# Performance work log

Hardware: AMD Instinct MI355X
Metric: run time of the kernel (lower is better)

## Reference

```python
import jax, jax.numpy as jnp
import numpy as np
from jax import lax

K = 5          # CARAFE kernel_size
S = 2          # scale_factor (downsample stride)
GROUP = 1      # mask groups
ENC_PAD = 1    # (encoder_kernel-1)*dilation//2 with encoder_kernel=3


def _conv2d(x, w, b, stride, padding, dilation=1):
    y = lax.conv_general_dilated(
        x, w, window_strides=(stride, stride),
        padding=[(padding, padding), (padding, padding)],
        rhs_dilation=(dilation, dilation),
        dimension_numbers=('NCHW', 'OIHW', 'NCHW'))
    return y + b[None, :, None, None]


def setup_inputs() -> dict:
    key = jax.random.key(0)
    k1, k2, k3 = jax.random.split(key, 3)
    B, C, H, W = 4, 256, 128, 128
    COMP = 64
    x = jax.random.normal(k1, (B, C, H, W), dtype=jnp.float32)
    # xavier-uniform-ish scale for compressor, std=0.001 for content encoder (as in init_weights)
    w1 = jax.random.normal(k2, (COMP, C, 1, 1), dtype=jnp.float32) * (1.0 / np.sqrt(C))
    b1 = jnp.zeros((COMP,), dtype=jnp.float32)
    w2 = jax.random.normal(k3, (K * K * GROUP, COMP, 3, 3), dtype=jnp.float32) * 0.001
    b2 = jnp.zeros((K * K * GROUP,), dtype=jnp.float32)
    return {"x": x, "w1": w1, "b1": b1, "w2": w2, "b2": b2}


def _carafe_forward(x, w1, b1, w2, b2):
    B, C, H, W = x.shape
    compressed = _conv2d(x, w1, b1, stride=1, padding=0)           # (B, 64, H, W)
    mask = _conv2d(compressed, w2, b2, stride=S, padding=ENC_PAD)   # (B, K*K*G, Ho, Wo)
    Ho, Wo = mask.shape[2], mask.shape[3]
    # kernel_normalizer: softmax over the K*K window per group
    mask = jax.nn.softmax(mask.reshape(B, GROUP, K * K, Ho, Wo), axis=2)
    # feature_reassemble: fused unfold * mask sum — accumulate per kernel tap to
    # avoid materializing the full (B, C, K*K, Ho, Wo) tensor.
    pad = K // 2
    x_pad = jnp.pad(x, ((0, 0), (0, 0), (pad, pad), (pad, pad)))
    Cg = C // GROUP
    out = jnp.zeros((B, GROUP, Cg, Ho, Wo), dtype=x.dtype)
    for i in range(K):
        for j in range(K):
            patch = x_pad[:, :, i:i + S * (Ho - 1) + 1:S, j:j + S * (Wo - 1) + 1:S]
            patch = patch.reshape(B, GROUP, Cg, Ho, Wo)
            out = out + patch * mask[:, :, i * K + j][:, :, None]
    return out.reshape(B, C, Ho, Wo)


def reference(x, w1, b1, w2, b2):
    return _carafe_forward(x, w1, b1, w2, b2)
```

## Files before the change

### kernel.cpp

```cpp
#include <hip/hip_runtime.h>
#include <math.h>

#define BN   4
#define CN   256
#define HN   128
#define WN   128
#define COMP 64
#define KK   25
#define HO   64
#define WO   64

#define TB_OFF    36864
#define PL_OFF    37120
#define PL_SLICE  (BN * HO * KK * 64)
#define XT_OFF    (PL_OFF + 2 * PL_SLICE)
#define WS_NEED   ((size_t)(XT_OFF + (size_t)BN * HN * WN * CN / 2) * 4)

typedef short v8s  __attribute__((ext_vector_type(8)));
typedef float v16f __attribute__((ext_vector_type(16)));

__device__ inline ushort f2bf(float f) {
  unsigned u = __float_as_uint(f);
  return (ushort)((u + 0x7fffu + ((u >> 16) & 1u)) >> 16);
}

__global__ __launch_bounds__(64) void compose_mfma(
    const float* __restrict__ w1, const float* __restrict__ b1,
    const float* __restrict__ w2, float* __restrict__ ws) {
  const int t = blockIdx.x, chunk = blockIdx.y;
  const int lane = threadIdx.x;
  const int m = lane & 31, half = lane >> 5;
  const int c0 = chunk * 16 + half * 8;
  float acc[8] = {0.f, 0.f, 0.f, 0.f, 0.f, 0.f, 0.f, 0.f};
  if (m < KK) {
    for (int k = 0; k < COMP; ++k) {
      float wv = w2[(size_t)(m * COMP + k) * 9 + t];
      const float* w1r = w1 + (size_t)k * CN + c0;
      float4 a = *(const float4*)w1r;
      float4 bq = *(const float4*)(w1r + 4);
      acc[0] += wv * a.x;  acc[1] += wv * a.y;
      acc[2] += wv * a.z;  acc[3] += wv * a.w;
      acc[4] += wv * bq.x; acc[5] += wv * bq.y;
      acc[6] += wv * bq.z; acc[7] += wv * bq.w;
    }
  }
  ushort* wA = (ushort*)ws;
  ushort pk[8];
#pragma unroll
  for (int j = 0; j < 8; ++j) pk[j] = f2bf(acc[j]);
  *(ushort4*)(wA + ((size_t)(t * 16 + chunk) * 64 + lane) * 8) =
      make_ushort4(pk[0], pk[1], pk[2], pk[3]);
  *(ushort4*)(wA + ((size_t)(t * 16 + chunk) * 64 + lane) * 8 + 4) =
      make_ushort4(pk[4], pk[5], pk[6], pk[7]);
  if (chunk == 0 && lane < KK) {
    float tbv = 0.f;
    for (int k = 0; k < COMP; ++k)
      tbv += w2[(size_t)(lane * COMP + k) * 9 + t] * b1[k];
    ws[TB_OFF + lane * 9 + t] = tbv;
  }
}

__global__ __launch_bounds__(256) void transpose_x(
    const float* __restrict__ x, float* __restrict__ ws) {
  __shared__ float st[64][65];
  const int wt = blockIdx.x & 1, ct = blockIdx.x >> 1;
  const int h = blockIdx.y, b = blockIdx.z;
  const int tid = threadIdx.x;
  const int w0 = wt * 64, c0 = ct * 64;
  {
    const int wl = tid & 63, cw = tid >> 6;
#pragma unroll
    for (int i = 0; i < 16; ++i) {
      int cl = cw * 16 + i;
      st[cl][wl] = x[((size_t)(b * CN + c0 + cl) * HN + h) * WN + w0 + wl];
    }
  }
  __syncthreads();
  ushort* xT = (ushort*)(ws + XT_OFF);
  const int cg = tid & 15, wl0 = tid >> 4;
#pragma unroll
  for (int wi = 0; wi < 4; ++wi) {
    int wl = wl0 + wi * 16;
    ushort4 o = make_ushort4(f2bf(st[cg * 4 + 0][wl]), f2bf(st[cg * 4 + 1][wl]),
                             f2bf(st[cg * 4 + 2][wl]), f2bf(st[cg * 4 + 3][wl]));
    *(ushort4*)(xT + ((size_t)((b * HN + h) * WN + w0 + wl)) * CN + c0 + cg * 4) = o;
  }
}

__global__ __launch_bounds__(64) void conv_mfma(
    const float* __restrict__ ws, float* __restrict__ pl) {
  const int wt = blockIdx.x & 1, z = blockIdx.x >> 1;
  const int ho = blockIdx.y, b = blockIdx.z;
  const int lane = threadIdx.x;
  const int n = lane & 31, half = lane >> 5;
  const int wo = wt * 32 + n;
  const ushort* xT = (const ushort*)(ws + XT_OFF);
  const ushort* wA = (const ushort*)ws;
  const int coff = z * 128 + half * 8;
  const v8s zero8 = {};
  v16f acc = {};

#pragma unroll
  for (int dr = 0; dr < 3; ++dr) {
    const int r = 2 * ho + dr - 1;
    if (r < 0) continue;
#pragma unroll
    for (int dc = 0; dc < 3; ++dc) {
      const int t = dr * 3 + dc;
      const int q = 2 * wo + dc - 1;
      const bool bad = q < 0;
      const int qc = bad ? 0 : q;
      const ushort* bp = xT + ((size_t)((b * HN + r) * WN + qc)) * CN + coff;
      const ushort* ap = wA + ((size_t)(t * 16 + z * 8) * 64 + lane) * 8;
      v8s bf[8], af[8];
#pragma unroll
      for (int cc = 0; cc < 8; ++cc) {
        bf[cc] = *(const v8s*)(bp + cc * 16);
        af[cc] = *(const v8s*)(ap + (size_t)cc * 512);
      }
      if (dc == 0) {
#pragma unroll
        for (int cc = 0; cc < 8; ++cc) bf[cc] = bad ? zero8 : bf[cc];
      }
#pragma unroll
      for (int cc = 0; cc < 8; ++cc)
        acc = __builtin_amdgcn_mfma_f32_32x32x16_bf16(af[cc], bf[cc], acc, 0, 0, 0);
    }
  }

  float* dst = pl + (size_t)z * PL_SLICE + ((size_t)(b * HO + ho) * KK) * 64 + wo;
#pragma unroll
  for (int rg = 0; rg < 16; ++rg) {
    int m = (rg & 3) + 8 * (rg >> 2) + 4 * half;
    if (m < KK) dst[(size_t)m * 64] = acc[rg];
  }
}

__global__ __launch_bounds__(1024, 4) void gather_kernel(
    const float* __restrict__ x, const float* __restrict__ b2,
    const float* __restrict__ tb, const float* __restrict__ pl,
    float* __restrict__ out) {
  const int ho  = blockIdx.x;
  const int b   = blockIdx.y;
  const int z   = blockIdx.z;
  const int tid = threadIdx.x;
  const int wo  = tid & 63;
  const int wv  = tid >> 6;
  const int c_base = __builtin_amdgcn_readfirstlane(z * (CN / 2) + wv * 8);

  __shared__ float sm[KK * 64];

  const float* __restrict__ xb = x + (size_t)(b * CN) * (HN * WN);
  const int col = 2 * wo;
  const float wok = (wo > 0) ? 1.f : 0.f;
  const float w63 = (wo < 63) ? 1.f : 0.f;

  float2 g[2][5];
  auto load_g = [&](int ci, float2* dst) {
    const float* xc = xb + (size_t)(c_base + ci) * (HN * WN);
#pragma unroll
    for (int i = 0; i < 5; ++i) {
      int r = 2 * ho - 2 + i;
      dst[i] = (r >= 0 && r < HN) ? *(const float2*)(xc + r * WN + col)
                                  : make_float2(0.f, 0.f);
    }
  };
  load_g(0, g[0]);
  load_g(1, g[1]);

  if (tid < 64) {
    const float vr0 = (ho > 0) ? 1.f : 0.f;
    const float vq0 = (wo > 0) ? 1.f : 0.f;
    const float* p0 = pl + (((size_t)b * HO + ho) * KK) * 64;
    const float* p1 = p0 + PL_SLICE;
    float logit[KK];
    float mx = -1e30f;
#pragma unroll
    for (int m = 0; m < KK; ++m) {
      const float* t9 = tb + m * 9;
      float l = b2[m]
              + vr0 * (vq0 * t9[0] + t9[1] + t9[2])
              +       (vq0 * t9[3] + t9[4] + t9[5])
              +       (vq0 * t9[6] + t9[7] + t9[8]);
      l += p0[m * 64 + wo] + p1[m * 64 + wo];
      logit[m] = l;
      mx = fmaxf(mx, l);
    }
    float s = 0.f;
#pragma unroll
    for (int m = 0; m < KK; ++m) {
      float e = __expf(logit[m] - mx);
      logit[m] = e;
      s += e;
    }
    float inv = 1.f / s;
#pragma unroll
    for (int m = 0; m < KK; ++m) sm[m * 64 + wo] = logit[m] * inv;
  }
  __syncthreads();

  float smr[KK];
#pragma unroll
  for (int m = 0; m < KK; ++m) smr[m] = sm[m * 64 + wo];

  for (int ci = 0; ci < 8; ++ci) {
    float2 v[5];
#pragma unroll
    for (int i = 0; i < 5; ++i) v[i] = g[ci & 1][i];
    if (ci + 2 < 8) load_g(ci + 2, g[ci & 1]);

    float acc2 = 0.f;
#pragma unroll
    for (int i = 0; i < 5; ++i) {
      float lx = wok * __shfl_up(v[i].x, 1, 64);
      float ly = wok * __shfl_up(v[i].y, 1, 64);
      float rx = w63 * __shfl_down(v[i].x, 1, 64);
      acc2 += lx * smr[i * 5 + 0] + ly * smr[i * 5 + 1]
            + v[i].x * smr[i * 5 + 2] + v[i].y * smr[i * 5 + 3]
            + rx * smr[i * 5 + 4];
    }
    out[(((size_t)(b * CN + c_base + ci)) * HO + ho) * WO + wo] = acc2;
  }
}

#define FB_WSTRIDE 240
#define FB_TB_OFF  (256 * FB_WSTRIDE)

__global__ __launch_bounds__(256) void compose_w_fb(
    const float* __restrict__ w1, const float* __restrict__ b1,
    const float* __restrict__ w2, float* __restrict__ ws) {
  int mt = blockIdx.x, c = threadIdx.x;
  float acc = 0.f;
#pragma unroll 8
  for (int k = 0; k < COMP; ++k)
    acc += w2[(size_t)(mt / 9 * COMP + k) * 9 + (mt % 9)] * w1[k * CN + c];
  ws[c * FB_WSTRIDE + mt] = acc;
  if (mt < FB_WSTRIDE - 225) ws[c * FB_WSTRIDE + 225 + mt] = 0.f;
  if (c == 0) {
    float tbv = 0.f;
    for (int k = 0; k < COMP; ++k)
      tbv += w2[(size_t)(mt / 9 * COMP + k) * 9 + (mt % 9)] * b1[k];
    ws[FB_TB_OFF + mt] = tbv;
  }
}

__global__ __launch_bounds__(1024, 4) void fused_fb(
    const float* __restrict__ x, const float* __restrict__ b2,
    const float* __restrict__ ws, float* __restrict__ out) {
  const int ho = blockIdx.x, b = blockIdx.y, tid = threadIdx.x;
  const int wo = tid & 63, wv = tid >> 6;
  const int c_base = __builtin_amdgcn_readfirstlane(wv * 16);
  const float* __restrict__ w2c = ws;
  const float* __restrict__ tb  = ws + FB_TB_OFF;
  __shared__ float red[8 * KK * 64];
  __shared__ float sm[KK * 64];
  const float* __restrict__ xb = x + (size_t)(b * CN) * (HN * WN);
  const int col = 2 * wo;
  float acc[KK];
#pragma unroll
  for (int m = 0; m < KK; ++m) acc[m] = 0.f;
  float2 xbuf[2][3];
  auto load_ch = [&](int ci, float2* dst) {
    const float* xc = xb + (size_t)(c_base + ci) * (HN * WN);
    dst[0] = (ho > 0) ? *(const float2*)(xc + (2 * ho - 1) * WN + col)
                      : make_float2(0.f, 0.f);
    dst[1] = *(const float2*)(xc + (2 * ho) * WN + col);
    dst[2] = *(const float2*)(xc + (2 * ho + 1) * WN + col);
  };
  load_ch(0, xbuf[0]);
  load_ch(1, xbuf[1]);
  const float wok = (wo > 0) ? 1.f : 0.f;
  for (int ci = 0; ci < 16; ++ci) {
    float2 r0 = xbuf[ci & 1][0], r1 = xbuf[ci & 1][1], r2 = xbuf[ci & 1][2];
    if (ci + 2 < 16) load_ch(ci + 2, xbuf[ci & 1]);
    float xv[9];
    xv[0] = wok * __shfl_up(r0.y, 1, 64); xv[1] = r0.x; xv[2] = r0.y;
    xv[3] = wok * __shfl_up(r1.y, 1, 64); xv[4] = r1.x; xv[5] = r1.y;
    xv[6] = wok * __shfl_up(r2.y, 1, 64); xv[7] = r2.x; xv[8] = r2.y;
    const float* __restrict__ wrow = w2c + (size_t)(c_base + ci) * FB_WSTRIDE;
#pragma unroll
    for (int m = 0; m < KK; ++m) {
      float a = acc[m];
#pragma unroll
      for (int t = 0; t < 9; ++t) a += wrow[m * 9 + t] * xv[t];
      acc[m] = a;
    }
  }
  float2 g[2][5];
  auto load_g = [&](int ci, float2* dst) {
    const float* xc = xb + (size_t)(c_base + ci) * (HN * WN);
#pragma unroll
    for (int i = 0; i < 5; ++i) {
      int r = 2 * ho - 2 + i;
      dst[i] = (r >= 0 && r < HN) ? *(const float2*)(xc + r * WN + col)
                                  : make_float2(0.f, 0.f);
    }
  };
  load_g(0, g[0]);
  load_g(1, g[1]);
  if (wv >= 8) {
#pragma unroll
    for (int m = 0; m < KK; ++m) red[((wv - 8) * KK + m) * 64 + wo] = acc[m];
  }
  __syncthreads();
  if (wv < 8) {
#pragma unroll
    for (int m = 0; m < KK; ++m) red[(wv * KK + m) * 64 + wo] += acc[m];
  }
  __syncthreads();
  if (wv < 4) {
#pragma unroll
    for (int m = 0; m < KK; ++m)
      red[(wv * KK + m) * 64 + wo] += red[((wv + 4) * KK + m) * 64 + wo];
  }
  __syncthreads();
  if (wv < 2) {
#pragma unroll
    for (int m = 0; m < KK; ++m)
      red[(wv * KK + m) * 64 + wo] += red[((wv + 2) * KK + m) * 64 + wo];
  }
  __syncthreads();
  if (tid < 64) {
    const float vr0 = (ho > 0) ? 1.f : 0.f;
    const float vq0 = (wo > 0) ? 1.f : 0.f;
    float logit[KK];
    float mx = -1e30f;
#pragma unroll
    for (int m = 0; m < KK; ++m) {
      const float* t9 = tb + m * 9;
      float l = b2[m]
              + vr0 * (vq0 * t9[0] + t9[1] + t9[2])
              +       (vq0 * t9[3] + t9[4] + t9[5])
              +       (vq0 * t9[6] + t9[7] + t9[8]);
      l += red[(0 * KK + m) * 64 + wo] + red[(1 * KK + m) * 64 + wo];
      logit[m] = l;
      mx = fmaxf(mx, l);
    }
    float s = 0.f;
#pragma unroll
    for (int m = 0; m < KK; ++m) {
      float e = __expf(logit[m] - mx);
      logit[m] = e;
      s += e;
    }
    float inv = 1.f / s;
#pragma unroll
    for (int m = 0; m < KK; ++m) sm[m * 64 + wo] = logit[m] * inv;
  }
  __syncthreads();
  float smr[KK];
#pragma unroll
  for (int m = 0; m < KK; ++m) smr[m] = sm[m * 64 + wo];
  const float w63 = (wo < 63) ? 1.f : 0.f;
  for (int ci = 0; ci < 16; ++ci) {
    float2 v[5];
#pragma unroll
    for (int i = 0; i < 5; ++i) v[i] = g[ci & 1][i];
    if (ci + 2 < 16) load_g(ci + 2, g[ci & 1]);
    float acc2 = 0.f;
#pragma unroll
    for (int i = 0; i < 5; ++i) {
      float lx = wok * __shfl_up(v[i].x, 1, 64);
      float ly = wok * __shfl_up(v[i].y, 1, 64);
      float rx = w63 * __shfl_down(v[i].x, 1, 64);
      acc2 += lx * smr[i * 5 + 0] + ly * smr[i * 5 + 1]
            + v[i].x * smr[i * 5 + 2] + v[i].y * smr[i * 5 + 3]
            + rx * smr[i * 5 + 4];
    }
    out[(((size_t)(b * CN + c_base + ci)) * HO + ho) * WO + wo] = acc2;
  }
}

extern "C" void kernel_launch(void* const* d_in, const int* in_sizes, int n_in,
                              void* d_out, int out_size, void* d_ws, size_t ws_size,
                              hipStream_t stream) {
  const float* x  = (const float*)d_in[0];
  const float* w1 = (const float*)d_in[1];
  const float* b1 = (const float*)d_in[2];
  const float* w2 = (const float*)d_in[3];
  const float* b2 = (const float*)d_in[4];
  float* out = (float*)d_out;
  float* ws  = (float*)d_ws;

  if (ws_size >= WS_NEED) {
    float* pl = ws + PL_OFF;
    hipLaunchKernelGGL(compose_mfma, dim3(9, 16), dim3(64), 0, stream,
                       w1, b1, w2, ws);
    hipLaunchKernelGGL(transpose_x, dim3(8, HN, BN), dim3(256), 0, stream,
                       x, ws);
    hipLaunchKernelGGL(conv_mfma, dim3(4, HO, BN), dim3(64), 0, stream,
                       ws, pl);
    hipLaunchKernelGGL(gather_kernel, dim3(HO, BN, 2), dim3(1024), 0, stream,
                       x, b2, ws + TB_OFF, pl, out);
  } else {
    hipLaunchKernelGGL(compose_w_fb, dim3(225), dim3(256), 0, stream,
                       w1, b1, w2, ws);
    hipLaunchKernelGGL(fused_fb, dim3(HO, BN), dim3(1024), 0, stream,
                       x, b2, ws, out);
  }
}
```

Baseline: 165.2 us.

## Split conv reduction into eight channel slices and move softmax to its own kernel

```diff
diff --git a/kernel.cpp b/kernel.cpp
--- a/kernel.cpp
+++ b/kernel.cpp
@@ -9,11 +9,13 @@
 #define KK   25
 #define HO   64
 #define WO   64
+#define NZC  8
 
 #define TB_OFF    36864
 #define PL_OFF    37120
 #define PL_SLICE  (BN * HO * KK * 64)
-#define XT_OFF    (PL_OFF + 2 * PL_SLICE)
+#define SM_OFF    (PL_OFF + NZC * PL_SLICE)
+#define XT_OFF    (SM_OFF + PL_SLICE)
 #define WS_NEED   ((size_t)(XT_OFF + (size_t)BN * HN * WN * CN / 2) * 4)
 
 typedef short v8s  __attribute__((ext_vector_type(8)));
@@ -96,7 +98,7 @@
   const int wo = wt * 32 + n;
   const ushort* xT = (const ushort*)(ws + XT_OFF);
   const ushort* wA = (const ushort*)ws;
-  const int coff = z * 128 + half * 8;
+  const int coff = z * 32 + half * 8;
   const v8s zero8 = {};
   v16f acc = {};
 
@@ -111,20 +113,14 @@
       const bool bad = q < 0;
       const int qc = bad ? 0 : q;
       const ushort* bp = xT + ((size_t)((b * HN + r) * WN + qc)) * CN + coff;
-      const ushort* ap = wA + ((size_t)(t * 16 + z * 8) * 64 + lane) * 8;
-      v8s bf[8], af[8];
-#pragma unroll
-      for (int cc = 0; cc < 8; ++cc) {
-        bf[cc] = *(const v8s*)(bp + cc * 16);
-        af[cc] = *(const v8s*)(ap + (size_t)cc * 512);
-      }
-      if (dc == 0) {
-#pragma unroll
-        for (int cc = 0; cc < 8; ++cc) bf[cc] = bad ? zero8 : bf[cc];
-      }
-#pragma unroll
-      for (int cc = 0; cc < 8; ++cc)
-        acc = __builtin_amdgcn_mfma_f32_32x32x16_bf16(af[cc], bf[cc], acc, 0, 0, 0);
+      const ushort* ap = wA + ((size_t)(t * 16 + z * 2) * 64 + lane) * 8;
+      v8s bf0 = *(const v8s*)bp;
+      v8s bf1 = *(const v8s*)(bp + 16);
+      v8s af0 = *(const v8s*)ap;
+      v8s af1 = *(const v8s*)(ap + 512);
+      if (dc == 0 && bad) { bf0 = zero8; bf1 = zero8; }
+      acc = __builtin_amdgcn_mfma_f32_32x32x16_bf16(af0, bf0, acc, 0, 0, 0);
+      acc = __builtin_amdgcn_mfma_f32_32x32x16_bf16(af1, bf1, acc, 0, 0, 0);
     }
   }
 
@@ -136,9 +132,44 @@
   }
 }
 
-__global__ __launch_bounds__(1024, 4) void gather_kernel(
-    const float* __restrict__ x, const float* __restrict__ b2,
-    const float* __restrict__ tb, const float* __restrict__ pl,
+__global__ __launch_bounds__(64) void softmax_kernel(
+    const float* __restrict__ b2, const float* __restrict__ tb,
+    const float* __restrict__ pl, float* __restrict__ sm) {
+  const int ho = blockIdx.x, b = blockIdx.y;
+  const int wo = threadIdx.x;
+  const float vr0 = (ho > 0) ? 1.f : 0.f;
+  const float vq0 = (wo > 0) ? 1.f : 0.f;
+  const float* base = pl + ((size_t)(b * HO + ho) * KK) * 64 + wo;
+  float logit[KK];
+  float mx = -1e30f;
+#pragma unroll
+  for (int m = 0; m < KK; ++m) {
+    const float* t9 = tb + m * 9;
+    float l = b2[m]
+            + vr0 * (vq0 * t9[0] + t9[1] + t9[2])
+            +       (vq0 * t9[3] + t9[4] + t9[5])
+            +       (vq0 * t9[6] + t9[7] + t9[8]);
+#pragma unroll
+    for (int s = 0; s < NZC; ++s)
+      l += base[(size_t)s * PL_SLICE + (size_t)m * 64];
+    logit[m] = l;
+    mx = fmaxf(mx, l);
+  }
+  float ssum = 0.f;
+#pragma unroll
+  for (int m = 0; m < KK; ++m) {
+    float e = __expf(logit[m] - mx);
+    logit[m] = e;
+    ssum += e;
+  }
+  float inv = 1.f / ssum;
+  float* dst = sm + ((size_t)(b * HO + ho) * KK) * 64 + wo;
+#pragma unroll
+  for (int m = 0; m < KK; ++m) dst[(size_t)m * 64] = logit[m] * inv;
+}
+
+__global__ __launch_bounds__(512) void gather_kernel(
+    const float* __restrict__ x, const float* __restrict__ sm,
     float* __restrict__ out) {
   const int ho  = blockIdx.x;
   const int b   = blockIdx.y;
@@ -146,9 +177,14 @@
   const int tid = threadIdx.x;
   const int wo  = tid & 63;
   const int wv  = tid >> 6;
-  const int c_base = __builtin_amdgcn_readfirstlane(z * (CN / 2) + wv * 8);
-
-  __shared__ float sm[KK * 64];
+  const int c_base = __builtin_amdgcn_readfirstlane(z * 64 + wv * 8);
+
+  float smr[KK];
+  {
+    const float* smp = sm + ((size_t)(b * HO + ho) * KK) * 64 + wo;
+#pragma unroll
+    for (int m = 0; m < KK; ++m) smr[m] = smp[(size_t)m * 64];
+  }
 
   const float* __restrict__ xb = x + (size_t)(b * CN) * (HN * WN);
   const int col = 2 * wo;
@@ -167,41 +203,6 @@
   };
   load_g(0, g[0]);
   load_g(1, g[1]);
-
-  if (tid < 64) {
-    const float vr0 = (ho > 0) ? 1.f : 0.f;
-    const float vq0 = (wo > 0) ? 1.f : 0.f;
-    const float* p0 = pl + (((size_t)b * HO + ho) * KK) * 64;
-    const float* p1 = p0 + PL_SLICE;
-    float logit[KK];
-    float mx = -1e30f;
-#pragma unroll
-    for (int m = 0; m < KK; ++m) {
-      const float* t9 = tb + m * 9;
-      float l = b2[m]
-              + vr0 * (vq0 * t9[0] + t9[1] + t9[2])
-              +       (vq0 * t9[3] + t9[4] + t9[5])
-              +       (vq0 * t9[6] + t9[7] + t9[8]);
-      l += p0[m * 64 + wo] + p1[m * 64 + wo];
-      logit[m] = l;
-      mx = fmaxf(mx, l);
-    }
-    float s = 0.f;
-#pragma unroll
-    for (int m = 0; m < KK; ++m) {
-      float e = __expf(logit[m] - mx);
-      logit[m] = e;
-      s += e;
-    }
-    float inv = 1.f / s;
-#pragma unroll
-    for (int m = 0; m < KK; ++m) sm[m * 64 + wo] = logit[m] * inv;
-  }
-  __syncthreads();
-
-  float smr[KK];
-#pragma unroll
-  for (int m = 0; m < KK; ++m) smr[m] = sm[m * 64 + wo];
 
   for (int ci = 0; ci < 8; ++ci) {
     float2 v[5];
@@ -384,14 +385,17 @@
 
   if (ws_size >= WS_NEED) {
     float* pl = ws + PL_OFF;
+    float* sm = ws + SM_OFF;
     hipLaunchKernelGGL(compose_mfma, dim3(9, 16), dim3(64), 0, stream,
                        w1, b1, w2, ws);
     hipLaunchKernelGGL(transpose_x, dim3(8, HN, BN), dim3(256), 0, stream,
                        x, ws);
-    hipLaunchKernelGGL(conv_mfma, dim3(4, HO, BN), dim3(64), 0, stream,
+    hipLaunchKernelGGL(conv_mfma, dim3(16, HO, BN), dim3(64), 0, stream,
                        ws, pl);
-    hipLaunchKernelGGL(gather_kernel, dim3(HO, BN, 2), dim3(1024), 0, stream,
-                       x, b2, ws + TB_OFF, pl, out);
+    hipLaunchKernelGGL(softmax_kernel, dim3(HO, BN), dim3(64), 0, stream,
+                       b2, ws + TB_OFF, pl, sm);
+    hipLaunchKernelGGL(gather_kernel, dim3(HO, BN, 4), dim3(512), 0, stream,
+                       x, sm, out);
   } else {
     hipLaunchKernelGGL(compose_w_fb, dim3(225), dim3(256), 0, stream,
                        w1, b1, w2, ws);
```

Result: slower. 214.5 us (+29.8%).
